# Performance work log

Measured on AMD Instinct MI355X. Metric: run time of the kernel, lower is better.

## Reference

```python
import jax, jax.numpy as jnp
import numpy as np

B, T, H, NH = 4, 2048, 1024, 16
HD = H // NH  # 64


def setup_inputs() -> dict:
    key = jax.random.key(0)
    ks = jax.random.split(key, 8)
    s = 1.0 / np.sqrt(H)
    return {
        "hidden_states": jax.random.normal(ks[0], (B, T, H), dtype=jnp.float32),
        "attention_mask": jnp.zeros((B, 1, 1, T), dtype=jnp.float32),
        "Wq": jax.random.normal(ks[1], (H, H), dtype=jnp.float32) * s,
        "bq": jax.random.normal(ks[2], (H,), dtype=jnp.float32) * 0.01,
        "Wk": jax.random.normal(ks[3], (H, H), dtype=jnp.float32) * s,
        "bk": jax.random.normal(ks[4], (H,), dtype=jnp.float32) * 0.01,
        "Wv": jax.random.normal(ks[5], (H, H), dtype=jnp.float32) * s,
        "bv": jax.random.normal(ks[6], (H,), dtype=jnp.float32) * 0.01,
    }


def _split_heads(x):
    # [b, t, h*d] -> [b, h, t, d]
    b, t, _ = x.shape
    return x.reshape(b, t, NH, HD).transpose(0, 2, 1, 3)


def reference(hidden_states, attention_mask, Wq, bq, Wk, bk, Wv, bv):
    q = _split_heads(hidden_states @ Wq.T + bq)
    k = _split_heads(hidden_states @ Wk.T + bk)
    v = _split_heads(hidden_states @ Wv.T + bv)
    scores = jnp.einsum('bhqd,bhkd->bhqk', q, k) / jnp.sqrt(jnp.float32(HD))
    t = q.shape[2]
    causal = jnp.triu(jnp.ones((t, t), dtype=scores.dtype), k=1)[None, None] * (-1e9)
    scores = scores + causal + attention_mask
    probs = jax.nn.softmax(scores, axis=-1)
    # module returns [b, h, t, d] (no merge back)
    return jnp.einsum('bhqk,bhkd->bhqd', probs, v)
```

## Files before the change

### kernel.cpp

```cpp
#include <hip/hip_runtime.h>
#include <hip/hip_bf16.h>


typedef float  f32x4 __attribute__((ext_vector_type(4)));
typedef short  s16x8 __attribute__((ext_vector_type(8)));
typedef unsigned short u16;

#define LOG2E 1.44269504088896340736f

__device__ __forceinline__ u16 f2bf(float f) {
  unsigned u = __float_as_uint(f);
  u += 0x7FFFu + ((u >> 16) & 1u);
  return (u16)(u >> 16);
}
__device__ __forceinline__ float bf2f(u16 v) {
  return __uint_as_float(((unsigned)v) << 16);
}
__device__ __forceinline__ float ex2(float x) {
#if __has_builtin(__builtin_amdgcn_exp2f)
  return __builtin_amdgcn_exp2f(x);
#else
  return exp2f(x);
#endif
}
__device__ __forceinline__ float rcp_(float x) {
#if __has_builtin(__builtin_amdgcn_rcpf)
  return __builtin_amdgcn_rcpf(x);
#else
  return 1.0f / x;
#endif
}
__device__ __forceinline__ unsigned cvtpk(float lo, float hi) {
  unsigned r;
  asm("v_cvt_pk_bf16_f32 %0, %1, %2" : "=v"(r) : "v"(lo), "v"(hi));
  return r;
}
__device__ __forceinline__ void bar() {
  asm volatile("" ::: "memory");
  __builtin_amdgcn_s_barrier();
  asm volatile("" ::: "memory");
}

#define GLOAD16(gp, lp)                                                          \
  __builtin_amdgcn_global_load_lds(                                              \
      (const __attribute__((address_space(1))) void*)(gp),                       \
      (__attribute__((address_space(3))) void*)(lp), 16, 0, 0)

#define MFMA(a, b, c) __builtin_amdgcn_mfma_f32_16x16x32_bf16((a), (b), (c), 0, 0, 0)

__global__ __launch_bounds__(256) void cvt_all(
    const float* __restrict__ hs, const float* __restrict__ wq,
    const float* __restrict__ wk, const float* __restrict__ wv,
    const float* __restrict__ maskp,
    u16* __restrict__ xo, u16* __restrict__ qo, u16* __restrict__ ko,
    u16* __restrict__ vo, u16* __restrict__ wm) {
  int b = blockIdx.x;
  const float* s;
  u16* d;
  size_t i;
  bool isw = false;
  if (b < 4096) { s = hs; d = xo; i = (size_t)b * 256 + threadIdx.x; }
  else if (b < 5632) {
    int w = (b - 4096) >> 9, r = (b - 4096) & 511;
    s = (w == 0) ? wq : (w == 1) ? wk : wv;
    d = (w == 0) ? qo : (w == 1) ? ko : vo;
    i = (size_t)r * 256 + threadIdx.x;
  } else {
    s = maskp; d = wm; i = (size_t)(b - 5632) * 256 + threadIdx.x;
    isw = true;
  }
  const float4* sp = (const float4*)s + i * 2;
  float4 a = sp[0], c = sp[1];
  s16x8 r8;
  if (isw) {
    r8[0] = f2bf(ex2(a.x * LOG2E)); r8[1] = f2bf(ex2(a.y * LOG2E));
    r8[2] = f2bf(ex2(a.z * LOG2E)); r8[3] = f2bf(ex2(a.w * LOG2E));
    r8[4] = f2bf(ex2(c.x * LOG2E)); r8[5] = f2bf(ex2(c.y * LOG2E));
    r8[6] = f2bf(ex2(c.z * LOG2E)); r8[7] = f2bf(ex2(c.w * LOG2E));
  } else {
    r8[0] = f2bf(a.x); r8[1] = f2bf(a.y); r8[2] = f2bf(a.z); r8[3] = f2bf(a.w);
    r8[4] = f2bf(c.x); r8[5] = f2bf(c.y); r8[6] = f2bf(c.z); r8[7] = f2bf(c.w);
  }
  *(s16x8*)(d + i * 8) = r8;
}

__global__ __launch_bounds__(512, 2) void qkv_gemm(
    const u16* __restrict__ Xb,
    const u16* __restrict__ Wqb, const u16* __restrict__ Wkb,
    const u16* __restrict__ Wvb,
    const float* __restrict__ bq, const float* __restrict__ bk,
    const float* __restrict__ bv, const u16* __restrict__ Wm,
    u16* __restrict__ Qo, u16* __restrict__ Ko, u16* __restrict__ Vto) {
  int bid0 = blockIdx.x;
  int bid  = (bid0 & 7) * 96 + (bid0 >> 3);
  int which = bid % 3;
  int rt = bid / 3;
  int mt = rt >> 3, nt = rt & 7;
  const u16* W = (which == 0) ? Wqb : (which == 1) ? Wkb : Wvb;
  const float* bias = (which == 0) ? bq : (which == 1) ? bk : bv;

  __shared__ __align__(16) char lds[98304];

  int tid = threadIdx.x;
  int lane = tid & 63, wid = tid >> 6;
  int q16 = lane & 15, g = lane >> 4;
  int wr = wid >> 1, wc = wid & 1;

  int srow = tid >> 3, sslot = tid & 7;
  int sw = (sslot ^ (srow & 7)) << 4;
  const char* Asrc = (const char*)Xb + (size_t)(mt * 256 + srow) * 2048 + sw;
  const char* Bsrc = (const char*)W  + (size_t)(nt * 128 + srow) * 2048 + sw;

  int slot0 = (g ^ (q16 & 7)) << 4;

#define STAGE_AB(tt, buf) do { size_t so = (size_t)(tt) * 128;                   \
    GLOAD16(Asrc + so,          lds + (buf) * 32768 + tid * 16);                 \
    GLOAD16(Asrc + so + 131072, lds + (buf) * 32768 + 8192 + tid * 16);          \
    GLOAD16(Asrc + so + 262144, lds + (buf) * 32768 + 16384 + tid * 16);         \
    GLOAD16(Asrc + so + 393216, lds + (buf) * 32768 + 24576 + tid * 16);         \
    GLOAD16(Bsrc + so,          lds + 65536 + (buf) * 16384 + tid * 16);         \
    GLOAD16(Bsrc + so + 131072, lds + 65536 + (buf) * 16384 + 8192 + tid * 16); } while (0)

#define LDA(FA, buf, mp) do {                                                    \
    const char* p_ = lds + (buf) * 32768 + (wr * 64 + (mp) * 32 + q16) * 128;    \
    FA[0] = *(const s16x8*)(p_ + slot0);                                         \
    FA[1] = *(const s16x8*)(p_ + (slot0 ^ 64));                                  \
    FA[2] = *(const s16x8*)(p_ + 2048 + slot0);                                  \
    FA[3] = *(const s16x8*)(p_ + 2048 + (slot0 ^ 64)); } while (0)

#define LDB(FB, buf) do {                                                        \
    const char* p_ = lds + 65536 + (buf) * 16384 + (wc * 64 + q16) * 128;        \
    FB[0] = *(const s16x8*)(p_ + slot0);                                         \
    FB[1] = *(const s16x8*)(p_ + (slot0 ^ 64));                                  \
    FB[2] = *(const s16x8*)(p_ + 2048 + slot0);                                  \
    FB[3] = *(const s16x8*)(p_ + 2048 + (slot0 ^ 64));                           \
    FB[4] = *(const s16x8*)(p_ + 4096 + slot0);                                  \
    FB[5] = *(const s16x8*)(p_ + 4096 + (slot0 ^ 64));                           \
    FB[6] = *(const s16x8*)(p_ + 6144 + slot0);                                  \
    FB[7] = *(const s16x8*)(p_ + 6144 + (slot0 ^ 64)); } while (0)

#define MM16(mlo, FA, FB) do {                                                   \
    _Pragma("unroll")                                                            \
    for (int n_ = 0; n_ < 4; ++n_) {                                             \
      acc[(mlo)][n_]     = MFMA(FA[0], FB[2 * n_],     acc[(mlo)][n_]);          \
      acc[(mlo)][n_]     = MFMA(FA[1], FB[2 * n_ + 1], acc[(mlo)][n_]);          \
      acc[(mlo) + 1][n_] = MFMA(FA[2], FB[2 * n_],     acc[(mlo) + 1][n_]);      \
      acc[(mlo) + 1][n_] = MFMA(FA[3], FB[2 * n_ + 1], acc[(mlo) + 1][n_]);      \
    } } while (0)

  STAGE_AB(0, 0);

  f32x4 acc[4][4] = {};
  s16x8 fA0[4], fA1[4], fB[8];

#pragma unroll 1
  for (int i = 0; i < 16; ++i) {
    int buf = i & 1;
    if (i < 15) {
      STAGE_AB(i + 1, buf ^ 1);
      asm volatile("s_waitcnt vmcnt(6)" ::: "memory");
    } else {
      asm volatile("s_waitcnt vmcnt(0)" ::: "memory");
    }
    bar();
    LDA(fA0, buf, 0);
    LDA(fA1, buf, 1);
    LDB(fB, buf);
    __builtin_amdgcn_s_setprio(1);
    MM16(0, fA0, fB);
    MM16(2, fA1, fB);
    __builtin_amdgcn_s_setprio(0);
    bar();
  }

  u16* tile = (u16*)(void*)lds + (size_t)wid * 64 * 72;
  int h0 = nt * 2 + wc;
  int m_base = mt * 256 + wr * 64;
  int bb = m_base >> 11;
  int t0 = m_base & 2047;

  if (which != 2) {
    float qsc = (which == 0) ? (0.125f * LOG2E) : 1.0f;
#pragma unroll
    for (int n = 0; n < 4; ++n) {
      float bvl = bias[h0 * 64 + n * 16 + q16];
#pragma unroll
      for (int m = 0; m < 4; ++m)
#pragma unroll
        for (int j = 0; j < 4; ++j)
          tile[(m * 16 + g * 4 + j) * 72 + n * 16 + q16] =
              f2bf((acc[m][n][j] + bvl) * qsc);
    }
  } else {
    const u16* wrow = Wm + (size_t)bb * 2048 + t0;
    float wv[4][4];
#pragma unroll
    for (int m = 0; m < 4; ++m)
#pragma unroll
      for (int j = 0; j < 4; ++j)
        wv[m][j] = bf2f(wrow[m * 16 + g * 4 + j]);
#pragma unroll
    for (int n = 0; n < 4; ++n) {
      float bvl = bias[h0 * 64 + n * 16 + q16];
#pragma unroll
      for (int m = 0; m < 4; ++m)
#pragma unroll
        for (int j = 0; j < 4; ++j)
          tile[(n * 16 + q16) * 72 + m * 16 + g * 4 + j] =
              f2bf((acc[m][n][j] + bvl) * wv[m][j]);
    }
  }
  asm volatile("" ::: "memory");

  const char* tb = (const char*)tile;
  int rl = lane >> 3, cb = (lane & 7) * 16;
  if (which != 2) {
    u16* Out = (which == 0) ? Qo : Ko;
    char* gbase = (char*)(Out + ((size_t)(bb * 16 + h0) * 2048 + t0) * 64);
#pragma unroll
    for (int c = 0; c < 8; ++c) {
      int row = rl + c * 8;
      s16x8 v = *(const s16x8*)(tb + row * 144 + cb);
      *(s16x8*)(gbase + row * 128 + cb) = v;
    }
  } else {
    char* gbase = (char*)Vto + ((size_t)(bb * 16 + h0) * 64) * 4096 + t0 * 2;
#pragma unroll
    for (int c = 0; c < 8; ++c) {
      int d = rl + c * 8;
      s16x8 v = *(const s16x8*)(tb + d * 144 + cb);
      *(s16x8*)(gbase + (size_t)d * 4096 + cb) = v;
    }
  }
#undef STAGE_AB
#undef LDA
#undef LDB
#undef MM16
}

__global__ __launch_bounds__(256, 2) void attn_fwd(
    const u16* __restrict__ Qw, const u16* __restrict__ Kw,
    const u16* __restrict__ Vtw, const u16* __restrict__ Wm,
    float* __restrict__ out) {
  int bid0 = blockIdx.x;
  int x = bid0 & 7, kk0 = bid0 >> 3;
  int r = kk0 >> 5, cc = kk0 & 31, u = cc & 7;
  int qt = r ? 7 - u : u;
  int bh = x * 8 + ((cc >> 3) | (r << 2));
  int qb = qt << 8;
  int tid = threadIdx.x;
  int lane = tid & 63, wid = tid >> 6;
  int q16 = lane & 15, g = lane >> 4;

  __shared__ __align__(16) char Ks[2][8192];
  __shared__ __align__(16) char Vs[2][8192];
  __shared__ __align__(16) u16 wl[2048];

  int qw0 = qb + wid * 64;
  size_t qr = (size_t)bh * 2048 + qw0 + q16;
  s16x8 qa[4][2];
#pragma unroll
  for (int h = 0; h < 4; ++h) {
    qa[h][0] = *(const s16x8*)(Qw + (qr + 16 * h) * 64 + g * 8);
    qa[h][1] = *(const s16x8*)(Qw + (qr + 16 * h) * 64 + 32 + g * 8);
  }

  int srow = tid >> 3;
  int sinner = (tid & 7) << 4;
  int fs = (srow & 7) ^ ((srow >> 1) & 4);
  int ssw = sinner ^ (fs << 4);
  const char* Kg = (const char*)Kw + ((size_t)bh * 2048 + srow) * 128 + ssw;
  const char* Vg = (const char*)Vtw + ((size_t)bh * 64 + srow) * 4096 + ssw;

  GLOAD16((const char*)Wm + (size_t)(bh >> 4) * 4096 + tid * 16,
          (char*)wl + tid * 16);
  GLOAD16(Kg, Ks[0] + tid * 16);
  GLOAD16(Kg + 4096, Ks[0] + tid * 16 + 4096);
  GLOAD16(Vg, Vs[0] + tid * 16);
  GLOAD16(Vg + 131072, Vs[0] + tid * 16 + 4096);
  __syncthreads();

  f32x4 o[4][4] = {};
  f32x4 lw[4] = {};

  int ntile = 4 * qt + 4;

  for (int kt = 0; kt < ntile; ++kt) {
    int cur = kt & 1;
    if (kt + 1 < ntile) {
      size_t kb2 = (size_t)(kt + 1) << 6;
      char* kd = Ks[cur ^ 1] + tid * 16;
      char* vd = Vs[cur ^ 1] + tid * 16;
      GLOAD16(Kg + kb2 * 128, kd);
      GLOAD16(Kg + kb2 * 128 + 4096, kd + 4096);
      GLOAD16(Vg + kb2 * 2, vd);
      GLOAD16(Vg + kb2 * 2 + 131072, vd + 4096);
      asm volatile("s_waitcnt vmcnt(4)" ::: "memory");
    } else {
      asm volatile("s_waitcnt vmcnt(0)" ::: "memory");
    }
    __builtin_amdgcn_s_barrier();
    asm volatile("" ::: "memory");

    int kb = kt << 6;
    const char* ksb = Ks[cur];
    const char* vsb = Vs[cur];

    if (64 * kt <= qw0 + 63) {
      bool causal = (64 * kt + 63 > qw0);
#pragma unroll
      for (int c = 0; c < 2; ++c) {
        f32x4 sA[2][4];
        __builtin_amdgcn_s_setprio(1);
#pragma unroll
        for (int t4 = 0; t4 < 2; ++t4) {
          int kk = 32 * c + ((q16 >> 2) << 3) + (t4 << 2) + (q16 & 3);
          int fk = (kk & 7) ^ ((kk >> 1) & 4);
          const char* krow = ksb + kk * 128;
          int in0 = (g * 16) ^ (fk << 4);
          s16x8 kf0 = *(const s16x8*)(krow + in0);
          s16x8 kf1 = *(const s16x8*)(krow + (in0 ^ 64));
#pragma unroll
          for (int h = 0; h < 4; ++h) {
            f32x4 sv = {0.f, 0.f, 0.f, 0.f};
            sv = MFMA(kf0, qa[h][0], sv);
            sv = MFMA(kf1, qa[h][1], sv);
            sA[t4][h] = sv;
          }
        }
        __builtin_amdgcn_s_setprio(0);

        s16x8 wf = *(const s16x8*)((const char*)wl + (kb + 32 * c + 8 * g) * 2);

        union { s16x8 v; unsigned u[4]; } pb[4];
#pragma unroll
        for (int h = 0; h < 4; ++h) {
          int qc = qw0 + 16 * h + q16;
#pragma unroll
          for (int t4 = 0; t4 < 2; ++t4) {
            float a0 = ex2(sA[t4][h][0]), a1 = ex2(sA[t4][h][1]);
            float a2 = ex2(sA[t4][h][2]), a3 = ex2(sA[t4][h][3]);
            if (causal) {
              int k0 = kb + 32 * c + 8 * g + 4 * t4;
              a0 = (k0 + 0 <= qc) ? a0 : 0.f;
              a1 = (k0 + 1 <= qc) ? a1 : 0.f;
              a2 = (k0 + 2 <= qc) ? a2 : 0.f;
              a3 = (k0 + 3 <= qc) ? a3 : 0.f;
            }
            pb[h].u[t4 * 2 + 0] = cvtpk(a0, a1);
            pb[h].u[t4 * 2 + 1] = cvtpk(a2, a3);
          }
        }

        __builtin_amdgcn_s_setprio(1);
#pragma unroll
        for (int dt = 0; dt < 4; ++dt) {
          int d = dt * 16 + q16;
          int fv = (d & 7) ^ ((d >> 1) & 4);
          s16x8 vf = *(const s16x8*)(vsb + d * 128 + ((64 * c + 16 * g) ^ (fv << 4)));
#pragma unroll
          for (int h = 0; h < 4; ++h)
            o[h][dt] = MFMA(vf, pb[h].v, o[h][dt]);
        }
#pragma unroll
        for (int h = 0; h < 4; ++h)
          lw[h] = MFMA(wf, pb[h].v, lw[h]);
        __builtin_amdgcn_s_setprio(0);
      }
    }
    __builtin_amdgcn_s_barrier();
  }

#pragma unroll
  for (int h = 0; h < 4; ++h) {
    float inv = rcp_(lw[h][0]);
    float* op = out + ((size_t)bh * 2048 + qw0 + 16 * h + q16) * 64 + g * 4;
#pragma unroll
    for (int dt = 0; dt < 4; ++dt)
      *(f32x4*)(op + dt * 16) = o[h][dt] * inv;
  }
}

extern "C" void kernel_launch(void* const* d_in, const int* in_sizes, int n_in,
                              void* d_out, int out_size, void* d_ws, size_t ws_size,
                              hipStream_t stream) {
  const float* hs   = (const float*)d_in[0];
  const float* mask = (const float*)d_in[1];
  const float* Wq   = (const float*)d_in[2];
  const float* bq   = (const float*)d_in[3];
  const float* Wk   = (const float*)d_in[4];
  const float* bk   = (const float*)d_in[5];
  const float* Wv   = (const float*)d_in[6];
  const float* bv   = (const float*)d_in[7];
  float* out = (float*)d_out;

  char* w = (char*)d_ws;
  u16* Xb  = (u16*)w; w += (size_t)8192 * 1024 * 2;
  u16* Wqb = (u16*)w; w += (size_t)1024 * 1024 * 2;
  u16* Wkb = (u16*)w; w += (size_t)1024 * 1024 * 2;
  u16* Wvb = (u16*)w; w += (size_t)1024 * 1024 * 2;
  u16* Qw  = (u16*)w; w += (size_t)8192 * 1024 * 2;
  u16* Kw  = (u16*)w; w += (size_t)8192 * 1024 * 2;
  u16* Vtw = (u16*)w; w += (size_t)8192 * 1024 * 2;
  u16* Wm  = (u16*)w; w += (size_t)8192 * 2;

  cvt_all<<<5636, 256, 0, stream>>>(hs, Wq, Wk, Wv, mask, Xb, Wqb, Wkb, Wvb, Wm);
  qkv_gemm<<<768, 512, 0, stream>>>(Xb, Wqb, Wkb, Wvb, bq, bk, bv, Wm, Qw, Kw, Vtw);
  attn_fwd<<<512, 256, 0, stream>>>(Qw, Kw, Vtw, Wm, out);
}
```

Baseline: 147.3 us.

## Pair causal query tiles per block and triple-buffer K/V loads

Each block now handles two 128-row query tiles, a heavy one (15-p) and a light one (p), so causal work per block is even instead of spread across 256-row tiles of very different length. Each wave owns 32 query rows instead of 64, which halves the per-wave accumulator registers. K/V staging moves from double to triple buffering with two tiles prefetched ahead. The trade-off is more total K/V reloads, a Q reload per phase, less MFMA reuse per K/V fragment, and more shared memory, which may limit occupancy.

```diff
diff --git a/kernel.cpp b/kernel.cpp
--- a/kernel.cpp
+++ b/kernel.cpp
@@ -243,27 +243,15 @@
     const u16* __restrict__ Vtw, const u16* __restrict__ Wm,
     float* __restrict__ out) {
   int bid0 = blockIdx.x;
-  int x = bid0 & 7, kk0 = bid0 >> 3;
-  int r = kk0 >> 5, cc = kk0 & 31, u = cc & 7;
-  int qt = r ? 7 - u : u;
-  int bh = x * 8 + ((cc >> 3) | (r << 2));
-  int qb = qt << 8;
+  int bid = (bid0 & 7) * 64 + (bid0 >> 3);
+  int bh = bid >> 3, p = bid & 7;
   int tid = threadIdx.x;
   int lane = tid & 63, wid = tid >> 6;
   int q16 = lane & 15, g = lane >> 4;
 
-  __shared__ __align__(16) char Ks[2][8192];
-  __shared__ __align__(16) char Vs[2][8192];
+  __shared__ __align__(16) char Ks[3][8192];
+  __shared__ __align__(16) char Vs[3][8192];
   __shared__ __align__(16) u16 wl[2048];
-
-  int qw0 = qb + wid * 64;
-  size_t qr = (size_t)bh * 2048 + qw0 + q16;
-  s16x8 qa[4][2];
-#pragma unroll
-  for (int h = 0; h < 4; ++h) {
-    qa[h][0] = *(const s16x8*)(Qw + (qr + 16 * h) * 64 + g * 8);
-    qa[h][1] = *(const s16x8*)(Qw + (qr + 16 * h) * 64 + 32 + g * 8);
-  }
 
   int srow = tid >> 3;
   int sinner = (tid & 7) << 4;
@@ -272,113 +260,129 @@
   const char* Kg = (const char*)Kw + ((size_t)bh * 2048 + srow) * 128 + ssw;
   const char* Vg = (const char*)Vtw + ((size_t)bh * 64 + srow) * 4096 + ssw;
 
+#define STAGE_T(kt, b) do {                                                      \
+    GLOAD16(Kg + (size_t)(kt) * 8192,        Ks[b] + tid * 16);                  \
+    GLOAD16(Kg + (size_t)(kt) * 8192 + 4096, Ks[b] + tid * 16 + 4096);           \
+    GLOAD16(Vg + (size_t)(kt) * 128,          Vs[b] + tid * 16);                 \
+    GLOAD16(Vg + (size_t)(kt) * 128 + 131072, Vs[b] + tid * 16 + 4096); } while (0)
+
   GLOAD16((const char*)Wm + (size_t)(bh >> 4) * 4096 + tid * 16,
           (char*)wl + tid * 16);
-  GLOAD16(Kg, Ks[0] + tid * 16);
-  GLOAD16(Kg + 4096, Ks[0] + tid * 16 + 4096);
-  GLOAD16(Vg, Vs[0] + tid * 16);
-  GLOAD16(Vg + 131072, Vs[0] + tid * 16 + 4096);
-  __syncthreads();
-
-  f32x4 o[4][4] = {};
-  f32x4 lw[4] = {};
-
-  int ntile = 4 * qt + 4;
-
-  for (int kt = 0; kt < ntile; ++kt) {
-    int cur = kt & 1;
-    if (kt + 1 < ntile) {
-      size_t kb2 = (size_t)(kt + 1) << 6;
-      char* kd = Ks[cur ^ 1] + tid * 16;
-      char* vd = Vs[cur ^ 1] + tid * 16;
-      GLOAD16(Kg + kb2 * 128, kd);
-      GLOAD16(Kg + kb2 * 128 + 4096, kd + 4096);
-      GLOAD16(Vg + kb2 * 2, vd);
-      GLOAD16(Vg + kb2 * 2 + 131072, vd + 4096);
-      asm volatile("s_waitcnt vmcnt(4)" ::: "memory");
-    } else {
-      asm volatile("s_waitcnt vmcnt(0)" ::: "memory");
-    }
-    __builtin_amdgcn_s_barrier();
-    asm volatile("" ::: "memory");
-
-    int kb = kt << 6;
-    const char* ksb = Ks[cur];
-    const char* vsb = Vs[cur];
-
-    if (64 * kt <= qw0 + 63) {
-      bool causal = (64 * kt + 63 > qw0);
-#pragma unroll
-      for (int c = 0; c < 2; ++c) {
-        f32x4 sA[2][4];
-        __builtin_amdgcn_s_setprio(1);
-#pragma unroll
-        for (int t4 = 0; t4 < 2; ++t4) {
-          int kk = 32 * c + ((q16 >> 2) << 3) + (t4 << 2) + (q16 & 3);
-          int fk = (kk & 7) ^ ((kk >> 1) & 4);
-          const char* krow = ksb + kk * 128;
-          int in0 = (g * 16) ^ (fk << 4);
-          s16x8 kf0 = *(const s16x8*)(krow + in0);
-          s16x8 kf1 = *(const s16x8*)(krow + (in0 ^ 64));
-#pragma unroll
-          for (int h = 0; h < 4; ++h) {
-            f32x4 sv = {0.f, 0.f, 0.f, 0.f};
-            sv = MFMA(kf0, qa[h][0], sv);
-            sv = MFMA(kf1, qa[h][1], sv);
-            sA[t4][h] = sv;
+
+  auto run_phase = [&](int qtl) {
+    int nt = 2 * qtl + 2;
+    int qw0 = (qtl << 7) + wid * 32;
+    size_t qr = (size_t)bh * 2048 + qw0 + q16;
+    s16x8 qa[2][2];
+#pragma unroll
+    for (int h = 0; h < 2; ++h) {
+      qa[h][0] = *(const s16x8*)(Qw + (qr + 16 * h) * 64 + g * 8);
+      qa[h][1] = *(const s16x8*)(Qw + (qr + 16 * h) * 64 + 32 + g * 8);
+    }
+    STAGE_T(0, 0);
+    STAGE_T(1, 1);
+
+    f32x4 o[2][4] = {};
+    f32x4 lw[2] = {};
+    int bc = 0;
+
+#pragma unroll 1
+    for (int kt = 0; kt < nt; ++kt) {
+      if (kt + 2 < nt) {
+        int bp = bc + 2; if (bp >= 3) bp -= 3;
+        STAGE_T(kt + 2, bp);
+        asm volatile("s_waitcnt vmcnt(8)" ::: "memory");
+      } else if (kt + 1 < nt) {
+        asm volatile("s_waitcnt vmcnt(4)" ::: "memory");
+      } else {
+        asm volatile("s_waitcnt vmcnt(0)" ::: "memory");
+      }
+      __builtin_amdgcn_s_barrier();
+      asm volatile("" ::: "memory");
+
+      if (64 * kt <= qw0 + 31) {
+        int kb = kt << 6;
+        const char* ksb = Ks[bc];
+        const char* vsb = Vs[bc];
+        bool causal = (64 * kt + 63 > qw0);
+#pragma unroll
+        for (int c = 0; c < 2; ++c) {
+          f32x4 sA[2][2];
+          __builtin_amdgcn_s_setprio(1);
+#pragma unroll
+          for (int t4 = 0; t4 < 2; ++t4) {
+            int kk = 32 * c + ((q16 >> 2) << 3) + (t4 << 2) + (q16 & 3);
+            int fk = (kk & 7) ^ ((kk >> 1) & 4);
+            const char* krow = ksb + kk * 128;
+            int in0 = (g * 16) ^ (fk << 4);
+            s16x8 kf0 = *(const s16x8*)(krow + in0);
+            s16x8 kf1 = *(const s16x8*)(krow + (in0 ^ 64));
+#pragma unroll
+            for (int h = 0; h < 2; ++h) {
+              f32x4 sv = {0.f, 0.f, 0.f, 0.f};
+              sv = MFMA(kf0, qa[h][0], sv);
+              sv = MFMA(kf1, qa[h][1], sv);
+              sA[t4][h] = sv;
+            }
           }
+          __builtin_amdgcn_s_setprio(0);
+
+          s16x8 wf = *(const s16x8*)((const char*)wl + (kb + 32 * c + 8 * g) * 2);
+
+          union { s16x8 v; unsigned u[4]; } pb[2];
+#pragma unroll
+          for (int h = 0; h < 2; ++h) {
+            int qc = qw0 + 16 * h + q16;
+#pragma unroll
+            for (int t4 = 0; t4 < 2; ++t4) {
+              float a0 = ex2(sA[t4][h][0]), a1 = ex2(sA[t4][h][1]);
+              float a2 = ex2(sA[t4][h][2]), a3 = ex2(sA[t4][h][3]);
+              if (causal) {
+                int k0 = kb + 32 * c + 8 * g + 4 * t4;
+                a0 = (k0 + 0 <= qc) ? a0 : 0.f;
+                a1 = (k0 + 1 <= qc) ? a1 : 0.f;
+                a2 = (k0 + 2 <= qc) ? a2 : 0.f;
+                a3 = (k0 + 3 <= qc) ? a3 : 0.f;
+              }
+              pb[h].u[t4 * 2 + 0] = cvtpk(a0, a1);
+              pb[h].u[t4 * 2 + 1] = cvtpk(a2, a3);
+            }
+          }
+
+          __builtin_amdgcn_s_setprio(1);
+#pragma unroll
+          for (int dt = 0; dt < 4; ++dt) {
+            int d = dt * 16 + q16;
+            int fv = (d & 7) ^ ((d >> 1) & 4);
+            s16x8 vf = *(const s16x8*)(vsb + d * 128 + ((64 * c + 16 * g) ^ (fv << 4)));
+#pragma unroll
+            for (int h = 0; h < 2; ++h)
+              o[h][dt] = MFMA(vf, pb[h].v, o[h][dt]);
+          }
+#pragma unroll
+          for (int h = 0; h < 2; ++h)
+            lw[h] = MFMA(wf, pb[h].v, lw[h]);
+          __builtin_amdgcn_s_setprio(0);
         }
-        __builtin_amdgcn_s_setprio(0);
-
-        s16x8 wf = *(const s16x8*)((const char*)wl + (kb + 32 * c + 8 * g) * 2);
-
-        union { s16x8 v; unsigned u[4]; } pb[4];
-#pragma unroll
-        for (int h = 0; h < 4; ++h) {
-          int qc = qw0 + 16 * h + q16;
-#pragma unroll
-          for (int t4 = 0; t4 < 2; ++t4) {
-            float a0 = ex2(sA[t4][h][0]), a1 = ex2(sA[t4][h][1]);
-            float a2 = ex2(sA[t4][h][2]), a3 = ex2(sA[t4][h][3]);
-            if (causal) {
-              int k0 = kb + 32 * c + 8 * g + 4 * t4;
-              a0 = (k0 + 0 <= qc) ? a0 : 0.f;
-              a1 = (k0 + 1 <= qc) ? a1 : 0.f;
-              a2 = (k0 + 2 <= qc) ? a2 : 0.f;
-              a3 = (k0 + 3 <= qc) ? a3 : 0.f;
-            }
-            pb[h].u[t4 * 2 + 0] = cvtpk(a0, a1);
-            pb[h].u[t4 * 2 + 1] = cvtpk(a2, a3);
-          }
-        }
-
-        __builtin_amdgcn_s_setprio(1);
-#pragma unroll
-        for (int dt = 0; dt < 4; ++dt) {
-          int d = dt * 16 + q16;
-          int fv = (d & 7) ^ ((d >> 1) & 4);
-          s16x8 vf = *(const s16x8*)(vsb + d * 128 + ((64 * c + 16 * g) ^ (fv << 4)));
-#pragma unroll
-          for (int h = 0; h < 4; ++h)
-            o[h][dt] = MFMA(vf, pb[h].v, o[h][dt]);
-        }
-#pragma unroll
-        for (int h = 0; h < 4; ++h)
-          lw[h] = MFMA(wf, pb[h].v, lw[h]);
-        __builtin_amdgcn_s_setprio(0);
       }
-    }
-    __builtin_amdgcn_s_barrier();
-  }
-
-#pragma unroll
-  for (int h = 0; h < 4; ++h) {
-    float inv = rcp_(lw[h][0]);
-    float* op = out + ((size_t)bh * 2048 + qw0 + 16 * h + q16) * 64 + g * 4;
-#pragma unroll
-    for (int dt = 0; dt < 4; ++dt)
-      *(f32x4*)(op + dt * 16) = o[h][dt] * inv;
-  }
+      __builtin_amdgcn_s_barrier();
+      asm volatile("" ::: "memory");
+      if (++bc >= 3) bc -= 3;
+    }
+
+#pragma unroll
+    for (int h = 0; h < 2; ++h) {
+      float inv = rcp_(lw[h][0]);
+      float* op = out + ((size_t)bh * 2048 + qw0 + 16 * h + q16) * 64 + g * 4;
+#pragma unroll
+      for (int dt = 0; dt < 4; ++dt)
+        *(f32x4*)(op + dt * 16) = o[h][dt] * inv;
+    }
+  };
+
+  run_phase(15 - p);
+  run_phase(p);
+#undef STAGE_T
 }
 
 extern "C" void kernel_launch(void* const* d_in, const int* in_sizes, int n_in,
```

After: 134.1 us. 9.0% less time.
